# Optimization experiments

Measured on AMD Instinct MI355X. Metric: run time of the kernel, lower is better.

## Reference

```python
import jax, jax.numpy as jnp
import numpy as np

N_NODES = 50000
N_EDGES = 600000
HIDDEN = 128
N_FEAT = 1
N_CLASSES = 2
N_GRAPHS = 500


def gcn_conv(x, W, b, src, dst, n_nodes):
    # PyG GCNConv: add self-loops, symmetric normalization deg^{-1/2} A_hat deg^{-1/2}, then XW + b
    h = x @ W  # [N, out]
    deg = jnp.zeros((n_nodes,), h.dtype).at[dst].add(1.0) + 1.0  # +1 for self-loop
    dinv = jax.lax.rsqrt(deg)
    norm = dinv[src] * dinv[dst]  # [E]
    agg = jax.ops.segment_sum(h[src] * norm[:, None], dst, num_segments=n_nodes)
    # self-loop contribution: norm_ii = dinv_i^2
    agg = agg + h * (dinv * dinv)[:, None]
    return agg + b


def setup_inputs() -> dict:
    key = jax.random.key(0)
    ks = jax.random.split(key, 12)
    x = jax.random.normal(ks[0], (N_NODES, N_FEAT), dtype=jnp.float32)
    edge_index = jax.random.randint(ks[1], (2, N_EDGES), 0, N_NODES, dtype=jnp.int64)
    batch = jnp.sort(jax.random.randint(ks[2], (N_NODES,), 0, N_GRAPHS, dtype=jnp.int64))

    def glorot(k, fan_in, fan_out):
        lim = np.sqrt(6.0 / (fan_in + fan_out)).astype(np.float32)
        return jax.random.uniform(k, (fan_in, fan_out), jnp.float32, -lim, lim)

    W1 = glorot(ks[3], N_FEAT, HIDDEN)
    b1 = jnp.zeros((HIDDEN,), jnp.float32)
    W2 = glorot(ks[4], HIDDEN, HIDDEN)
    b2 = jnp.zeros((HIDDEN,), jnp.float32)
    W3 = glorot(ks[5], HIDDEN, HIDDEN)
    b3 = jnp.zeros((HIDDEN,), jnp.float32)
    Wlin = glorot(ks[6], HIDDEN, N_CLASSES)
    blin = jnp.zeros((N_CLASSES,), jnp.float32)
    return {"x": x, "W1": W1, "b1": b1, "W2": W2, "b2": b2, "W3": W3,
            "b3": b3, "Wlin": Wlin, "blin": blin,
            "edge_index": edge_index, "batch": batch}


def reference(x, W1, b1, W2, b2, W3, b3, Wlin, blin, edge_index, batch):
    src, dst = edge_index[0], edge_index[1]
    n = x.shape[0]
    h = jax.nn.relu(gcn_conv(x, W1, b1, src, dst, n))
    h = jax.nn.relu(gcn_conv(h, W2, b2, src, dst, n))
    h = gcn_conv(h, W3, b3, src, dst, n)
    # global mean pool over graphs
    sums = jax.ops.segment_sum(h, batch, num_segments=N_GRAPHS)
    counts = jax.ops.segment_sum(jnp.ones((n,), h.dtype), batch, num_segments=N_GRAPHS)
    pooled = sums / jnp.maximum(counts, 1.0)[:, None]  # [G, HIDDEN]
    # dropout is identity in eval mode
    return pooled @ Wlin + blin  # [G, N_CLASSES]
```

## Files before the change

### kernel.cpp

```cpp
#include <hip/hip_runtime.h>
#include <hip/hip_bf16.h>

#define N_NODES 50000
#define N_EDGES 600000
#define HID     128
#define NG      500
#define NB_SCAN 196
#define MAXDEG  48
#define ECAP    768
#define EB4     587


__global__ void k_ellfill(const int* __restrict__ src, const int* __restrict__ dst,
                          int* __restrict__ cnt, int* __restrict__ ell_t,
                          const float* __restrict__ W3, const float* __restrict__ Wlin,
                          const float* __restrict__ b3, const float* __restrict__ blin,
                          float* __restrict__ w3buf) {
    if (blockIdx.x == EB4 - 1) {
        int t = threadIdx.x;
        int k = t >> 1, j = t & 1;
        float acc = 0.f;
        for (int m = 0; m < 128; m++) acc += W3[k * 128 + m] * Wlin[m * 2 + j];
        w3buf[k * 2 + j] = acc;
        if (t < 2) {
            float c = 0.f;
            for (int m = 0; m < 128; m++) c += b3[m] * Wlin[m * 2 + t];
            w3buf[256 + t] = c + blin[t];
            w3buf[258 + t] = blin[t];
        }
        return;
    }
    int base = blockIdx.x * 1024 + threadIdx.x;
    #pragma unroll
    for (int u = 0; u < 4; u++) {
        int e = base + u * 256;
        if (e < N_EDGES) {
            int d = dst[e];
            int p = atomicAdd(&cnt[d], 1);
            if (p < MAXDEG) ell_t[p * N_NODES + d] = src[e];
        }
    }
}

__global__ void k_nodeprep(const int* __restrict__ cnt, const float* __restrict__ x,
                           float* __restrict__ dinv, float* __restrict__ xd) {
    int i = blockIdx.x * 256 + threadIdx.x;
    if (i < N_NODES) {
        float di = rsqrtf((float)cnt[i] + 1.0f);
        dinv[i] = di;
        xd[i] = x[i] * di;
    }
}

__global__ void k_s1d(const float* __restrict__ x, const float* __restrict__ xd,
                      const float* __restrict__ dinv, const int* __restrict__ cnt,
                      const int* __restrict__ ell_t, float2* __restrict__ s1d) {
    int tid = blockIdx.x * 256 + threadIdx.x;
    int i = tid >> 2, sub = tid & 3;
    if (i >= N_NODES) return;
    int c = min(cnt[i], MAXDEG);
    float acc = 0.f;
    for (int p = sub; p < c; p += 4) acc += xd[ell_t[p * N_NODES + i]];
    acc += __shfl_xor(acc, 1);
    acc += __shfl_xor(acc, 2);
    if (sub == 0) {
        float di = dinv[i];
        float2 r = {x[i] * di * di + acc * di, di};
        s1d[i] = r;
    }
}


__global__ __launch_bounds__(256, 8) void k_gemm_fused(const float2* __restrict__ s1d,
                                                       const int* __restrict__ cnt,
                                                       const int* __restrict__ ell_t,
                                                       const float* __restrict__ W1,
                                                       const float* __restrict__ b1,
                                                       const float* __restrict__ W2,
                                                       const float* __restrict__ b2,
                                                       const float* __restrict__ w3buf,
                                                       float* __restrict__ zd) {
    __shared__ float HsT[128 * 32];
    __shared__ float2 sjd_sh[ECAP];
    __shared__ int cnt_sh[32];
    __shared__ int pref_sh[33];
    __shared__ int maxc_sh;
    int t = threadIdx.x;
    int r0 = blockIdx.x * 32;
    int lane = t & 31, grp = t >> 5;

    if (t < 32) {
        int i = r0 + t;
        int c = (i < N_NODES) ? min(cnt[i], MAXDEG) : 0;
        cnt_sh[t] = c;
        int inc = c, mx = c;
        for (int o = 1; o < 32; o <<= 1) {
            int u = __shfl_up(inc, o);
            if (t >= o) inc += u;
            mx = max(mx, __shfl_xor(mx, o));
        }
        pref_sh[t] = inc - c;
        if (t == 31) { pref_sh[32] = inc; maxc_sh = mx; }
    }
    __syncthreads();
    int total = pref_sh[32];
    int maxc  = maxc_sh;
    bool fast = (total <= ECAP);
    if (fast) {
        for (int slot = t; slot < 32 * maxc; slot += 256) {
            int p = slot >> 5, ln = slot & 31;
            if (p < cnt_sh[ln]) {
                int j = ell_t[p * N_NODES + r0 + ln];
                sjd_sh[pref_sh[ln] + p] = s1d[j];
            }
        }
    }
    __syncthreads();

    float w1r[16], b1r[16];
    #pragma unroll
    for (int kk = 0; kk < 16; kk++) { w1r[kk] = W1[grp * 16 + kk]; b1r[kk] = b1[grp * 16 + kk]; }

    float ga[16];
    #pragma unroll
    for (int kk = 0; kk < 16; kk++) ga[kk] = 0.f;
    int node = r0 + lane;
    if (node < N_NODES) {
        float2 sd = s1d[node];
        float di = sd.y, wself = sd.y * sd.y;
        #pragma unroll
        for (int kk = 0; kk < 16; kk++) ga[kk] = fmaxf(sd.x * w1r[kk] + b1r[kk], 0.f) * wself;
        int c = cnt_sh[lane];
        if (fast) {
            const float2* myrow = &sjd_sh[pref_sh[lane]];
            int p = 0;
            for (; p + 3 < c; p += 4) {
                float2 s0 = myrow[p], s1v = myrow[p+1], s2 = myrow[p+2], s3 = myrow[p+3];
                float wj0 = s0.y * di, wj1 = s1v.y * di, wj2 = s2.y * di, wj3 = s3.y * di;
                #pragma unroll
                for (int kk = 0; kk < 16; kk++) {
                    ga[kk] += fmaxf(s0.x  * w1r[kk] + b1r[kk], 0.f) * wj0
                            + fmaxf(s1v.x * w1r[kk] + b1r[kk], 0.f) * wj1
                            + fmaxf(s2.x  * w1r[kk] + b1r[kk], 0.f) * wj2
                            + fmaxf(s3.x  * w1r[kk] + b1r[kk], 0.f) * wj3;
                }
            }
            for (; p < c; p++) {
                float2 sj = myrow[p];
                float wj = sj.y * di;
                #pragma unroll
                for (int kk = 0; kk < 16; kk++)
                    ga[kk] += fmaxf(sj.x * w1r[kk] + b1r[kk], 0.f) * wj;
            }
        } else {
            for (int p = 0; p < c; p++) {
                float2 sj = s1d[ell_t[p * N_NODES + node]];
                float wj = sj.y * di;
                #pragma unroll
                for (int kk = 0; kk < 16; kk++)
                    ga[kk] += fmaxf(sj.x * w1r[kk] + b1r[kk], 0.f) * wj;
            }
        }
    }
    #pragma unroll
    for (int kk = 0; kk < 16; kk++) HsT[(grp * 16 + kk) * 32 + lane] = ga[kk];
    __syncthreads();

    int col = (t & 31) * 4;
    int row = (t >> 5) * 4;
    float a[4][4] = {};
    #pragma unroll 4
    for (int k = 0; k < 128; k++) {
        float4 w = *(const float4*)&W2[k * 128 + col];
        float4 h = *(float4*)&HsT[k * 32 + row];
        a[0][0] += h.x * w.x; a[0][1] += h.x * w.y; a[0][2] += h.x * w.z; a[0][3] += h.x * w.w;
        a[1][0] += h.y * w.x; a[1][1] += h.y * w.y; a[1][2] += h.y * w.z; a[1][3] += h.y * w.w;
        a[2][0] += h.z * w.x; a[2][1] += h.z * w.y; a[2][2] += h.z * w.z; a[2][3] += h.z * w.w;
        a[3][0] += h.w * w.x; a[3][1] += h.w * w.y; a[3][2] += h.w * w.z; a[3][3] += h.w * w.w;
    }

    float b2r[4], w0r[4], w1rr[4];
    #pragma unroll
    for (int c = 0; c < 4; c++) {
        b2r[c] = b2[col + c];
        w0r[c] = w3buf[(col + c) * 2 + 0];
        w1rr[c] = w3buf[(col + c) * 2 + 1];
    }
    #pragma unroll
    for (int r = 0; r < 4; r++) {
        float p0 = 0.f, p1 = 0.f;
        #pragma unroll
        for (int c = 0; c < 4; c++) {
            float v0 = fmaxf(a[r][c] + b2r[c], 0.f);
            p0 += v0 * w0r[c];
            p1 += v0 * w1rr[c];
        }
        for (int o = 1; o < 32; o <<= 1) { p0 += __shfl_xor(p0, o); p1 += __shfl_xor(p1, o); }
        int rg = r0 + row + r;
        if ((t & 31) == 0 && rg < N_NODES) {
            float dr = s1d[rg].y;
            zd[rg * 2 + 0] = p0 * dr;
            zd[rg * 2 + 1] = p1 * dr;
        }
    }
}


__global__ void k_aggz(const float* __restrict__ zd, const int* __restrict__ cnt,
                       const int* __restrict__ ell_t, const float* __restrict__ dinv,
                       float2* __restrict__ az) {
    int tid = blockIdx.x * 256 + threadIdx.x;
    int i = tid >> 2, sub = tid & 3;
    if (i >= N_NODES) return;
    const float2* Z = (const float2*)zd;
    int c = min(cnt[i], MAXDEG);
    float a0 = 0.f, a1 = 0.f;
    for (int p = sub; p < c; p += 4) {
        float2 zj = Z[ell_t[p * N_NODES + i]];
        a0 += zj.x; a1 += zj.y;
    }
    a0 += __shfl_xor(a0, 1); a1 += __shfl_xor(a1, 1);
    a0 += __shfl_xor(a0, 2); a1 += __shfl_xor(a1, 2);
    if (sub == 0) {
        float di = dinv[i];
        float2 zi = Z[i];
        float2 r = {(zi.x + a0) * di, (zi.y + a1) * di};
        az[i] = r;
    }
}


__global__ __launch_bounds__(64) void k_final(const float2* __restrict__ az,
                                              const int* __restrict__ batch,
                                              const float* __restrict__ w3buf,
                                              float* __restrict__ out) {
    int g = blockIdx.x;
    int lane = threadIdx.x;
    int lo = 0, hi = N_NODES;
    while (lo < hi) { int mid = (lo + hi) >> 1; if (batch[mid] < g) lo = mid + 1; else hi = mid; }
    int start = lo;
    hi = N_NODES;
    while (lo < hi) { int mid = (lo + hi) >> 1; if (batch[mid] < g + 1) lo = mid + 1; else hi = mid; }
    int end = lo;
    float a0 = 0.f, a1 = 0.f;
    for (int n = start + lane; n < end; n += 64) {
        float2 v = az[n];
        a0 += v.x; a1 += v.y;
    }
    for (int o = 32; o; o >>= 1) { a0 += __shfl_xor(a0, o); a1 += __shfl_xor(a1, o); }
    if (lane == 0) {
        if (end > start) {
            float inv = 1.0f / (float)(end - start);
            out[g * 2 + 0] = a0 * inv + w3buf[256];
            out[g * 2 + 1] = a1 * inv + w3buf[257];
        } else {
            out[g * 2 + 0] = w3buf[258];
            out[g * 2 + 1] = w3buf[259];
        }
    }
}


extern "C" void kernel_launch(void* const* d_in, const int* in_sizes, int n_in,
                              void* d_out, int out_size, void* d_ws, size_t ws_size,
                              hipStream_t stream) {
    const float* x    = (const float*)d_in[0];
    const float* W1   = (const float*)d_in[1];
    const float* b1   = (const float*)d_in[2];
    const float* W2   = (const float*)d_in[3];
    const float* b2   = (const float*)d_in[4];
    const float* W3   = (const float*)d_in[5];
    const float* b3   = (const float*)d_in[6];
    const float* Wlin = (const float*)d_in[7];
    const float* blin = (const float*)d_in[8];
    const int*   eidx = (const int*)d_in[9];
    const int*   batch= (const int*)d_in[10];
    const int* esrc = eidx;
    const int* edst = eidx + N_EDGES;
    float* out = (float*)d_out;

    char* w = (char*)d_ws;
    size_t off = 0;
    auto alloc = [&](size_t bytes) { size_t o = off; off = (off + bytes + 255) & ~(size_t)255; return o; };
    int*   cnt    = (int*)  (w + alloc(N_NODES * 4));
    int*   ell_t  = (int*)  (w + alloc((size_t)N_NODES * MAXDEG * 4));
    float* dinv   = (float*)(w + alloc(N_NODES * 4));
    float* xd     = (float*)(w + alloc(N_NODES * 4));
    float2* s1d   = (float2*)(w + alloc((size_t)N_NODES * 8));
    float* w3buf  = (float*)(w + alloc(260 * 4));
    float* zd     = (float*)(w + alloc((size_t)N_NODES * 2 * 4));
    float2* az    = (float2*)(w + alloc((size_t)N_NODES * 8));

    const int QB = (N_NODES * 4 + 255) / 256;
    hipMemsetAsync(cnt, 0, N_NODES * 4, stream);
    k_ellfill<<<EB4, 256, 0, stream>>>(esrc, edst, cnt, ell_t, W3, Wlin, b3, blin, w3buf);
    k_nodeprep<<<NB_SCAN, 256, 0, stream>>>(cnt, x, dinv, xd);
    k_s1d<<<QB, 256, 0, stream>>>(x, xd, dinv, cnt, ell_t, s1d);
    k_gemm_fused<<<(N_NODES + 31) / 32, 256, 0, stream>>>(s1d, cnt, ell_t,
                                                          W1, b1, W2, b2, w3buf, zd);
    k_aggz<<<QB, 256, 0, stream>>>(zd, cnt, ell_t, dinv, az);
    k_final<<<NG, 64, 0, stream>>>(az, batch, w3buf, out);
}
```

Baseline: 177.3 us.

## Use split-bf16 MFMA for fused layer-2 GEMM and precompute graph start offsets

Replaces the scalar FP32 32x128x128 GEMM in the fused kernel with bf16 MFMA 16x16x32 instructions. It uses a hi/lo split (three MFMAs per tile) to keep near-FP32 accuracy. W2 is pre-split and swizzled into MFMA fragment layout by an extra block of the edge-fill kernel, which also precomputes per-graph start offsets so the final pooling kernel skips its binary searches. The shared-memory tile is cut from fp32 to two bf16 arrays and ECAP is reduced, and an LDS reduction across waves is added for the Wlin projection. The trade-off is 3x MFMA work and some extra precision risk in exchange for using matrix cores.

New measurement: 160.0 us. -9.7%, faster.

```diff
diff --git a/kernel.cpp b/kernel.cpp
--- a/kernel.cpp
+++ b/kernel.cpp
@@ -1,5 +1,4 @@
 #include <hip/hip_runtime.h>
-#include <hip/hip_bf16.h>
 
 #define N_NODES 50000
 #define N_EDGES 600000
@@ -7,26 +6,56 @@
 #define NG      500
 #define NB_SCAN 196
 #define MAXDEG  48
-#define ECAP    768
-#define EB4     587
+#define ECAP    664
+#define EBLK    586
+
+typedef __attribute__((ext_vector_type(8))) short short8;
+typedef __attribute__((ext_vector_type(4))) float f32x4;
+
+static __device__ __forceinline__ ushort f2bf(float f) {
+    uint u = __float_as_uint(f);
+    return (ushort)((u + 0x7fffu + ((u >> 16) & 1u)) >> 16);
+}
+static __device__ __forceinline__ float bf2f(ushort h) {
+    return __uint_as_float(((uint)h) << 16);
+}
 
 
 __global__ void k_ellfill(const int* __restrict__ src, const int* __restrict__ dst,
                           int* __restrict__ cnt, int* __restrict__ ell_t,
-                          const float* __restrict__ W3, const float* __restrict__ Wlin,
-                          const float* __restrict__ b3, const float* __restrict__ blin,
-                          float* __restrict__ w3buf) {
-    if (blockIdx.x == EB4 - 1) {
+                          const float* __restrict__ W2, const float* __restrict__ W3,
+                          const float* __restrict__ Wlin, const float* __restrict__ b3,
+                          const float* __restrict__ blin, const int* __restrict__ batch,
+                          float* __restrict__ w3buf, ushort* __restrict__ w2fh,
+                          ushort* __restrict__ w2fl, int* __restrict__ starts) {
+    if (blockIdx.x >= EBLK) {
         int t = threadIdx.x;
-        int k = t >> 1, j = t & 1;
-        float acc = 0.f;
-        for (int m = 0; m < 128; m++) acc += W3[k * 128 + m] * Wlin[m * 2 + j];
-        w3buf[k * 2 + j] = acc;
-        if (t < 2) {
-            float c = 0.f;
-            for (int m = 0; m < 128; m++) c += b3[m] * Wlin[m * 2 + t];
-            w3buf[256 + t] = c + blin[t];
-            w3buf[258 + t] = blin[t];
+        if (blockIdx.x == EBLK) {
+            int k = t >> 1, j = t & 1;
+            float acc = 0.f;
+            for (int m = 0; m < 128; m++) acc += W3[k * 128 + m] * Wlin[m * 2 + j];
+            w3buf[k * 2 + j] = acc;
+            if (t < 2) {
+                float c = 0.f;
+                for (int m = 0; m < 128; m++) c += b3[m] * Wlin[m * 2 + t];
+                w3buf[256 + t] = c + blin[t];
+                w3buf[258 + t] = blin[t];
+            }
+        } else {
+            for (int idx = t; idx < 16384; idx += 256) {
+                int nt = idx >> 11, kt = (idx >> 9) & 3, ln = (idx >> 3) & 63, i = idx & 7;
+                int k = kt * 32 + (ln >> 4) * 8 + i;
+                int col = nt * 16 + (ln & 15);
+                float v = W2[k * 128 + col];
+                ushort h = f2bf(v);
+                w2fh[idx] = h;
+                w2fl[idx] = f2bf(v - bf2f(h));
+            }
+            for (int g = t; g <= NG; g += 256) {
+                int lo = 0, hi = N_NODES;
+                while (lo < hi) { int mid = (lo + hi) >> 1; if (batch[mid] < g) lo = mid + 1; else hi = mid; }
+                starts[g] = lo;
+            }
         }
         return;
     }
@@ -76,11 +105,14 @@
                                                        const int* __restrict__ ell_t,
                                                        const float* __restrict__ W1,
                                                        const float* __restrict__ b1,
-                                                       const float* __restrict__ W2,
+                                                       const ushort* __restrict__ w2fh,
+                                                       const ushort* __restrict__ w2fl,
                                                        const float* __restrict__ b2,
                                                        const float* __restrict__ w3buf,
+                                                       const float* __restrict__ dinv,
                                                        float* __restrict__ zd) {
-    __shared__ float HsT[128 * 32];
+    __shared__ __align__(16) ushort Hhi[32 * 136];
+    __shared__ __align__(16) ushort Hlo[32 * 136];
     __shared__ float2 sjd_sh[ECAP];
     __shared__ int cnt_sh[32];
     __shared__ int pref_sh[33];
@@ -163,45 +195,107 @@
         }
     }
     #pragma unroll
-    for (int kk = 0; kk < 16; kk++) HsT[(grp * 16 + kk) * 32 + lane] = ga[kk];
+    for (int kk = 0; kk < 16; kk += 2) {
+        int ch = grp * 16 + kk;
+        ushort h0 = f2bf(ga[kk]);      ushort l0 = f2bf(ga[kk]     - bf2f(h0));
+        ushort h1v = f2bf(ga[kk + 1]); ushort l1v = f2bf(ga[kk + 1] - bf2f(h1v));
+        *(uint*)&Hhi[lane * 136 + ch] = (uint)h0 | ((uint)h1v << 16);
+        *(uint*)&Hlo[lane * 136 + ch] = (uint)l0 | ((uint)l1v << 16);
+    }
     __syncthreads();
 
-    int col = (t & 31) * 4;
-    int row = (t >> 5) * 4;
-    float a[4][4] = {};
-    #pragma unroll 4
-    for (int k = 0; k < 128; k++) {
-        float4 w = *(const float4*)&W2[k * 128 + col];
-        float4 h = *(float4*)&HsT[k * 32 + row];
-        a[0][0] += h.x * w.x; a[0][1] += h.x * w.y; a[0][2] += h.x * w.z; a[0][3] += h.x * w.w;
-        a[1][0] += h.y * w.x; a[1][1] += h.y * w.y; a[1][2] += h.y * w.z; a[1][3] += h.y * w.w;
-        a[2][0] += h.z * w.x; a[2][1] += h.z * w.y; a[2][2] += h.z * w.z; a[2][3] += h.z * w.w;
-        a[3][0] += h.w * w.x; a[3][1] += h.w * w.y; a[3][2] += h.w * w.z; a[3][3] += h.w * w.w;
-    }
-
-    float b2r[4], w0r[4], w1rr[4];
-    #pragma unroll
-    for (int c = 0; c < 4; c++) {
-        b2r[c] = b2[col + c];
-        w0r[c] = w3buf[(col + c) * 2 + 0];
-        w1rr[c] = w3buf[(col + c) * 2 + 1];
-    }
-    #pragma unroll
-    for (int r = 0; r < 4; r++) {
-        float p0 = 0.f, p1 = 0.f;
-        #pragma unroll
-        for (int c = 0; c < 4; c++) {
-            float v0 = fmaxf(a[r][c] + b2r[c], 0.f);
-            p0 += v0 * w0r[c];
-            p1 += v0 * w1rr[c];
-        }
-        for (int o = 1; o < 32; o <<= 1) { p0 += __shfl_xor(p0, o); p1 += __shfl_xor(p1, o); }
-        int rg = r0 + row + r;
-        if ((t & 31) == 0 && rg < N_NODES) {
-            float dr = s1d[rg].y;
-            zd[rg * 2 + 0] = p0 * dr;
-            zd[rg * 2 + 1] = p1 * dr;
-        }
+    int wv = t >> 6, l = t & 63;
+    int l15 = l & 15, lk = l >> 4;
+    f32x4 acc00 = {0.f,0.f,0.f,0.f}, acc01 = {0.f,0.f,0.f,0.f};
+    f32x4 acc10 = {0.f,0.f,0.f,0.f}, acc11 = {0.f,0.f,0.f,0.f};
+    const short8* Bh = (const short8*)w2fh;
+    const short8* Bl = (const short8*)w2fl;
+    #pragma unroll
+    for (int kt = 0; kt < 4; kt++) {
+        int ao = l15 * 136 + kt * 32 + lk * 8;
+        short8 ah0 = *(const short8*)&Hhi[ao];
+        short8 ah1 = *(const short8*)&Hhi[ao + 16 * 136];
+        short8 al0 = *(const short8*)&Hlo[ao];
+        short8 al1 = *(const short8*)&Hlo[ao + 16 * 136];
+        {
+            int ng = 2 * wv;
+            short8 bh = Bh[(ng * 4 + kt) * 64 + l];
+            short8 bl = Bl[(ng * 4 + kt) * 64 + l];
+            acc00 = __builtin_amdgcn_mfma_f32_16x16x32_bf16(ah0, bh, acc00, 0, 0, 0);
+            acc00 = __builtin_amdgcn_mfma_f32_16x16x32_bf16(ah0, bl, acc00, 0, 0, 0);
+            acc00 = __builtin_amdgcn_mfma_f32_16x16x32_bf16(al0, bh, acc00, 0, 0, 0);
+            acc10 = __builtin_amdgcn_mfma_f32_16x16x32_bf16(ah1, bh, acc10, 0, 0, 0);
+            acc10 = __builtin_amdgcn_mfma_f32_16x16x32_bf16(ah1, bl, acc10, 0, 0, 0);
+            acc10 = __builtin_amdgcn_mfma_f32_16x16x32_bf16(al1, bh, acc10, 0, 0, 0);
+        }
+        {
+            int ng = 2 * wv + 1;
+            short8 bh = Bh[(ng * 4 + kt) * 64 + l];
+            short8 bl = Bl[(ng * 4 + kt) * 64 + l];
+            acc01 = __builtin_amdgcn_mfma_f32_16x16x32_bf16(ah0, bh, acc01, 0, 0, 0);
+            acc01 = __builtin_amdgcn_mfma_f32_16x16x32_bf16(ah0, bl, acc01, 0, 0, 0);
+            acc01 = __builtin_amdgcn_mfma_f32_16x16x32_bf16(al0, bh, acc01, 0, 0, 0);
+            acc11 = __builtin_amdgcn_mfma_f32_16x16x32_bf16(ah1, bh, acc11, 0, 0, 0);
+            acc11 = __builtin_amdgcn_mfma_f32_16x16x32_bf16(ah1, bl, acc11, 0, 0, 0);
+            acc11 = __builtin_amdgcn_mfma_f32_16x16x32_bf16(al1, bh, acc11, 0, 0, 0);
+        }
+    }
+
+    float p0[2][4], p1[2][4];
+    #pragma unroll
+    for (int mt = 0; mt < 2; mt++)
+        #pragma unroll
+        for (int r = 0; r < 4; r++) { p0[mt][r] = 0.f; p1[mt][r] = 0.f; }
+    {
+        int colg = (2 * wv) * 16 + l15;
+        float b2c = b2[colg], w0 = w3buf[colg * 2], w1c = w3buf[colg * 2 + 1];
+        #pragma unroll
+        for (int r = 0; r < 4; r++) {
+            float v0 = fmaxf(acc00[r] + b2c, 0.f);
+            float v1 = fmaxf(acc10[r] + b2c, 0.f);
+            p0[0][r] += v0 * w0; p1[0][r] += v0 * w1c;
+            p0[1][r] += v1 * w0; p1[1][r] += v1 * w1c;
+        }
+    }
+    {
+        int colg = (2 * wv + 1) * 16 + l15;
+        float b2c = b2[colg], w0 = w3buf[colg * 2], w1c = w3buf[colg * 2 + 1];
+        #pragma unroll
+        for (int r = 0; r < 4; r++) {
+            float v0 = fmaxf(acc01[r] + b2c, 0.f);
+            float v1 = fmaxf(acc11[r] + b2c, 0.f);
+            p0[0][r] += v0 * w0; p1[0][r] += v0 * w1c;
+            p0[1][r] += v1 * w0; p1[1][r] += v1 * w1c;
+        }
+    }
+    #pragma unroll
+    for (int o = 1; o < 16; o <<= 1) {
+        #pragma unroll
+        for (int mt = 0; mt < 2; mt++)
+            #pragma unroll
+            for (int r = 0; r < 4; r++) {
+                p0[mt][r] += __shfl_xor(p0[mt][r], o);
+                p1[mt][r] += __shfl_xor(p1[mt][r], o);
+            }
+    }
+    float* zpart = (float*)sjd_sh;
+    if (l15 == 0) {
+        #pragma unroll
+        for (int mt = 0; mt < 2; mt++)
+            #pragma unroll
+            for (int r = 0; r < 4; r++) {
+                int row = mt * 16 + lk * 4 + r;
+                zpart[(wv * 32 + row) * 2 + 0] = p0[mt][r];
+                zpart[(wv * 32 + row) * 2 + 1] = p1[mt][r];
+            }
+    }
+    __syncthreads();
+    if (t < 64) {
+        int row = t >> 1, o = t & 1;
+        float s = zpart[row * 2 + o] + zpart[(32 + row) * 2 + o]
+                + zpart[(64 + row) * 2 + o] + zpart[(96 + row) * 2 + o];
+        int rg = r0 + row;
+        if (rg < N_NODES) zd[rg * 2 + o] = s * dinv[rg];
     }
 }
 
@@ -231,17 +325,12 @@
 
 
 __global__ __launch_bounds__(64) void k_final(const float2* __restrict__ az,
-                                              const int* __restrict__ batch,
+                                              const int* __restrict__ starts,
                                               const float* __restrict__ w3buf,
                                               float* __restrict__ out) {
     int g = blockIdx.x;
     int lane = threadIdx.x;
-    int lo = 0, hi = N_NODES;
-    while (lo < hi) { int mid = (lo + hi) >> 1; if (batch[mid] < g) lo = mid + 1; else hi = mid; }
-    int start = lo;
-    hi = N_NODES;
-    while (lo < hi) { int mid = (lo + hi) >> 1; if (batch[mid] < g + 1) lo = mid + 1; else hi = mid; }
-    int end = lo;
+    int start = starts[g], end = starts[g + 1];
     float a0 = 0.f, a1 = 0.f;
     for (int n = start + lane; n < end; n += 64) {
         float2 v = az[n];
@@ -290,14 +379,19 @@
     float* w3buf  = (float*)(w + alloc(260 * 4));
     float* zd     = (float*)(w + alloc((size_t)N_NODES * 2 * 4));
     float2* az    = (float2*)(w + alloc((size_t)N_NODES * 8));
+    ushort* w2fh  = (ushort*)(w + alloc(16384 * 2));
+    ushort* w2fl  = (ushort*)(w + alloc(16384 * 2));
+    int*   starts = (int*)  (w + alloc((NG + 4) * 4));
 
     const int QB = (N_NODES * 4 + 255) / 256;
     hipMemsetAsync(cnt, 0, N_NODES * 4, stream);
-    k_ellfill<<<EB4, 256, 0, stream>>>(esrc, edst, cnt, ell_t, W3, Wlin, b3, blin, w3buf);
+    k_ellfill<<<EBLK + 2, 256, 0, stream>>>(esrc, edst, cnt, ell_t, W2, W3, Wlin, b3, blin,
+                                            batch, w3buf, w2fh, w2fl, starts);
     k_nodeprep<<<NB_SCAN, 256, 0, stream>>>(cnt, x, dinv, xd);
     k_s1d<<<QB, 256, 0, stream>>>(x, xd, dinv, cnt, ell_t, s1d);
     k_gemm_fused<<<(N_NODES + 31) / 32, 256, 0, stream>>>(s1d, cnt, ell_t,
-                                                          W1, b1, W2, b2, w3buf, zd);
+                                                          W1, b1, w2fh, w2fl, b2, w3buf,
+                                                          dinv, zd);
     k_aggz<<<QB, 256, 0, stream>>>(zd, cnt, ell_t, dinv, az);
-    k_final<<<NG, 64, 0, stream>>>(az, batch, w3buf, out);
-}
+    k_final<<<NG, 64, 0, stream>>>(az, starts, w3buf, out);
+}
```
